# Optimization experiments

Measured on AMD Instinct MI355X. Metric: run time of the kernel, lower is better.

The kernel has to match this reference:

```python
import jax, jax.numpy as jnp
import numpy as np

EMBED_DIM = 1024
NUM_HEADS = 16
HEAD_DIM = EMBED_DIM // NUM_HEADS


def setup_inputs() -> dict:
    key = jax.random.key(0)
    ks = jax.random.split(key, 9)
    B, T, C = 4, 2048, EMBED_DIM
    s = 1.0 / np.sqrt(C)
    return {
        "x": jax.random.normal(ks[0], (B, T, C), jnp.float32),
        "Wq": jax.random.normal(ks[1], (C, C), jnp.float32) * s,
        "bq": jnp.zeros((C,), jnp.float32),
        "Wk": jax.random.normal(ks[2], (C, C), jnp.float32) * s,
        "bk": jnp.zeros((C,), jnp.float32),
        "Wv": jax.random.normal(ks[3], (C, C), jnp.float32) * s,
        "bv": jnp.zeros((C,), jnp.float32),
        "Wo": jax.random.normal(ks[4], (C, C), jnp.float32) * s,
        "bo": jnp.zeros((C,), jnp.float32),
    }


def reference(x, Wq, bq, Wk, bk, Wv, bv, Wo, bo):
    B, T, C = x.shape
    H, D = NUM_HEADS, HEAD_DIM
    # projections (torch Linear: y = x @ W.T + b; here weights stored as [in, out])
    q = (x @ Wq + bq).reshape(B, T, H, D).transpose(0, 2, 1, 3)  # [B,H,T,D]
    k = (x @ Wk + bk).reshape(B, T, H, D).transpose(0, 2, 1, 3)
    v = (x @ Wv + bv).reshape(B, T, H, D).transpose(0, 2, 1, 3)
    scores = jnp.einsum("bhqd,bhkd->bhqk", q, k) / jnp.sqrt(jnp.float32(D))
    causal = jnp.tril(jnp.ones((T, T), bool))
    scores = jnp.where(causal, scores, -jnp.inf)
    attn = jax.nn.softmax(scores, axis=-1)
    out = jnp.einsum("bhqk,bhkd->bhqd", attn, v)  # [B,H,T,D]
    out = out.transpose(0, 2, 1, 3).reshape(B, T, C)
    return out @ Wo + bo
```

## Files before the change

### kernel.cpp

```cpp
#include <hip/hip_runtime.h>
#include <hip/hip_bf16.h>
#include <math.h>

typedef __hip_bfloat16 bf16_t;
typedef __attribute__((ext_vector_type(8))) short short8;
typedef __attribute__((ext_vector_type(4))) float floatx4;

#define T_SEQ 2048
#define NB    4
#define NH    16
#define HD    64
#define C_DIM 1024
#define M_ROWS (NB * T_SEQ)

#define Q_SCALE 0.18033688011f

__device__ __forceinline__ void load_lds16(const bf16_t* g, bf16_t* l) {
    __builtin_amdgcn_global_load_lds(
        (const __attribute__((address_space(1))) void*)g,
        (__attribute__((address_space(3))) void*)l,
        16, 0, 0);
}

__device__ __forceinline__ floatx4 mfma16(short8 a, short8 b, floatx4 c) {
    return __builtin_amdgcn_mfma_f32_16x16x32_bf16(a, b, c, 0, 0, 0);
}

__global__ void convert_x_kernel(const float* __restrict__ x, bf16_t* __restrict__ xb) {
    int i = blockIdx.x * 256 + threadIdx.x;
    float4 v = reinterpret_cast<const float4*>(x)[i];
    union { bf16_t h[4]; short4 s4; } u;
    u.h[0] = __float2bfloat16(v.x);
    u.h[1] = __float2bfloat16(v.y);
    u.h[2] = __float2bfloat16(v.z);
    u.h[3] = __float2bfloat16(v.w);
    reinterpret_cast<short4*>(xb)[i] = u.s4;
}

__global__ void transpose_cvt_kernel(const float* __restrict__ W0, const float* __restrict__ W1,
                                     const float* __restrict__ W2, const float* __restrict__ W3,
                                     bf16_t* __restrict__ O0, bf16_t* __restrict__ O1,
                                     bf16_t* __restrict__ O2, bf16_t* __restrict__ O3) {
    const float* W = (blockIdx.z == 0) ? W0 : (blockIdx.z == 1) ? W1 : (blockIdx.z == 2) ? W2 : W3;
    bf16_t*      O = (blockIdx.z == 0) ? O0 : (blockIdx.z == 1) ? O1 : (blockIdx.z == 2) ? O2 : O3;
    __shared__ float tile[32][33];
    int bx = blockIdx.x * 32, by = blockIdx.y * 32;
    int tx = threadIdx.x, ty = threadIdx.y;
#pragma unroll
    for (int j = 0; j < 32; j += 8)
        tile[ty + j][tx] = W[(size_t)(by + ty + j) * C_DIM + bx + tx];
    __syncthreads();
#pragma unroll
    for (int j = 0; j < 32; j += 8)
        O[(size_t)(bx + ty + j) * C_DIM + by + tx] = __float2bfloat16(tile[tx][ty + j]);
}

__device__ __forceinline__ void gemm_mainloop(const bf16_t* __restrict__ Ablk,
                                              const bf16_t* __restrict__ Bblk,
                                              bf16_t* As, bf16_t* Bs,
                                              floatx4 acc[4][4], int wave, int lane) {
    int lr = lane & 15, lq = lane >> 4;
    int wr = (wave >> 1) * 64, wc = (wave & 1) * 64;
    for (int kt = 0; kt < C_DIM; kt += 64) {
#pragma unroll
        for (int j = 0; j < 4; ++j) {
            int chunk = j * 256 + wave * 64 + lane;
            int r = chunk >> 3, ps = chunk & 7;
            int c = ((ps ^ (r & 7)) * 8);
            load_lds16(Ablk + (size_t)r * C_DIM + kt + c, As + chunk * 8);
            load_lds16(Bblk + (size_t)r * C_DIM + kt + c, Bs + chunk * 8);
        }
        __syncthreads();
#pragma unroll
        for (int kk = 0; kk < 2; ++kk) {
            short8 af[4], bfr[4];
            int psw = ((kk * 4 + lq) ^ (lr & 7)) * 8;
#pragma unroll
            for (int m = 0; m < 4; ++m)
                af[m] = *reinterpret_cast<const short8*>(As + (wr + m * 16 + lr) * 64 + psw);
#pragma unroll
            for (int n = 0; n < 4; ++n)
                bfr[n] = *reinterpret_cast<const short8*>(Bs + (wc + n * 16 + lr) * 64 + psw);
#pragma unroll
            for (int m = 0; m < 4; ++m)
#pragma unroll
                for (int n = 0; n < 4; ++n)
                    acc[m][n] = mfma16(af[m], bfr[n], acc[m][n]);
        }
        __syncthreads();
    }
}

__global__ __launch_bounds__(256, 3) void gemm_qkv_kernel(
    const bf16_t* __restrict__ xb,
    const bf16_t* __restrict__ WqT, const bf16_t* __restrict__ WkT, const bf16_t* __restrict__ WvT,
    const float* __restrict__ bq, const float* __restrict__ bk, const float* __restrict__ bv,
    bf16_t* __restrict__ Q, bf16_t* __restrict__ K, bf16_t* __restrict__ Vt) {
    __shared__ bf16_t As[128 * 64];
    __shared__ bf16_t Bs[128 * 64];
    int tid = threadIdx.x, wave = tid >> 6, lane = tid & 63;

    int f    = (int)blockIdx.x + ((int)blockIdx.y << 3) + ((int)blockIdx.z << 9);
    int xcd  = f & 7;
    int s    = f >> 3;
    int rloc = s & 7;
    int t2   = s >> 3;
    int colp = t2 & 7;
    int wsel = t2 >> 3;
    int row0 = (xcd * 8 + rloc) * 128;
    int col0 = colp * 128;

    const bf16_t* Wt  = (wsel == 0) ? WqT : (wsel == 1) ? WkT : WvT;
    const float* bias = (wsel == 0) ? bq : (wsel == 1) ? bk : bv;

    floatx4 acc[4][4] = {};
    gemm_mainloop(xb + (size_t)row0 * C_DIM, Wt + (size_t)col0 * C_DIM, As, Bs, acc, wave, lane);

    int lr = lane & 15, lq = lane >> 4;
    int wr = (wave >> 1) * 64, wc = (wave & 1) * 64;

    if (wsel == 2) {
#pragma unroll
        for (int nt = 0; nt < 4; ++nt) {
            int col = col0 + wc + nt * 16 + lr;
            float bvv = bias[col];
            int h = col >> 6, d = col & 63;
#pragma unroll
            for (int m = 0; m < 4; ++m) {
                int rowg0 = row0 + wr + m * 16 + lq * 4;
                int b = rowg0 >> 11, t0 = rowg0 & (T_SEQ - 1);
                union { bf16_t h4[4]; short4 s4; } u;
#pragma unroll
                for (int r = 0; r < 4; ++r)
                    u.h4[r] = __float2bfloat16(acc[m][nt][r] + bvv);
                *reinterpret_cast<short4*>(
                    &Vt[((size_t)((b * NH + h) * HD + d)) * T_SEQ + t0]) = u.s4;
            }
        }
    } else {
        float scale = (wsel == 0) ? Q_SCALE : 1.0f;
        bf16_t* outp = (wsel == 0) ? Q : K;
#pragma unroll
        for (int nt = 0; nt < 4; ++nt) {
            int col = col0 + wc + nt * 16 + lr;
            float bvv = bias[col];
            int h = col >> 6, d = col & 63;
#pragma unroll
            for (int m = 0; m < 4; ++m) {
#pragma unroll
                for (int r = 0; r < 4; ++r) {
                    int rowg = row0 + wr + m * 16 + lq * 4 + r;
                    int b = rowg >> 11, t = rowg & (T_SEQ - 1);
                    float val = (acc[m][nt][r] + bvv) * scale;
                    outp[((size_t)((b * NH + h) * T_SEQ + t)) * HD + d] =
                        __float2bfloat16(val);
                }
            }
        }
    }
}

__global__ __launch_bounds__(256, 2) void attn_kernel(
    const bf16_t* __restrict__ Q, const bf16_t* __restrict__ K,
    const bf16_t* __restrict__ Vt, bf16_t* __restrict__ ctx) {
    __shared__ __align__(16) bf16_t Ks[2][64 * 64];
    __shared__ __align__(16) bf16_t Vs[2][64 * 64];
    __shared__ __align__(16) unsigned short Ps[128 * 64];
    int tid = threadIdx.x, w = tid >> 6, lane = tid & 63;
    int lr = lane & 15, lq = lane >> 4;
    int xcd = (int)blockIdx.x;
    int y   = (int)blockIdx.y;
    int bh  = xcd * 8 + (y & 7);
    int qp  = y >> 3;
    int b = bh >> 4, h = bh & 15;

    const bf16_t* Kbase = K  + (size_t)bh * T_SEQ * HD;
    const bf16_t* Vbase = Vt + (size_t)bh * HD * T_SEQ;

#pragma unroll 1
    for (int pass = 0; pass < 2; ++pass) {
        int qt = pass ? qp : (15 - qp);
        int q0 = qt * 128;
        int ktiles = 2 * qt + 2;
        const bf16_t* Qbase = Q + ((size_t)bh * T_SEQ + q0) * HD;

#pragma unroll
        for (int cc = 0; cc < 2; ++cc) {
            int ch = tid + cc * 256;
            int r = ch >> 3, ps = ch & 7;
            int c = ((ps ^ (r & 7)) * 8);
            load_lds16(Kbase + (size_t)r * HD + c, Ks[0] + ch * 8);
            load_lds16(Vbase + (size_t)r * T_SEQ + c, Vs[0] + ch * 8);
        }

        short8 qf[2][2];
#pragma unroll
        for (int g = 0; g < 2; ++g)
#pragma unroll
            for (int kk = 0; kk < 2; ++kk)
                qf[g][kk] = *reinterpret_cast<const short8*>(
                    Qbase + (size_t)(w * 32 + g * 16 + lr) * HD + kk * 32 + lq * 8);

        floatx4 o[2][4] = {};
        float lpart[2][4] = {};
        int buf = 0;

        for (int it = 0; it < ktiles; ++it) {
            int kt0 = it * 64;
            __syncthreads();

            if (it + 1 < ktiles) {
                int nk0 = kt0 + 64;
#pragma unroll
                for (int cc = 0; cc < 2; ++cc) {
                    int ch = tid + cc * 256;
                    int r = ch >> 3, ps = ch & 7;
                    int c = ((ps ^ (r & 7)) * 8);
                    load_lds16(Kbase + (size_t)(nk0 + r) * HD + c, Ks[buf ^ 1] + ch * 8);
                    load_lds16(Vbase + (size_t)r * T_SEQ + nk0 + c, Vs[buf ^ 1] + ch * 8);
                }
            }

            const bf16_t* Kc = Ks[buf];
            const bf16_t* Vc = Vs[buf];

            floatx4 s[2][4] = {};
            short8 kf[4][2];
#pragma unroll
            for (int kk = 0; kk < 2; ++kk) {
                int psw = ((kk * 4 + lq) ^ (lr & 7)) * 8;
#pragma unroll
                for (int n = 0; n < 4; ++n)
                    kf[n][kk] = *reinterpret_cast<const short8*>(Kc + (n * 16 + lr) * 64 + psw);
            }
#pragma unroll
            for (int g = 0; g < 2; ++g)
#pragma unroll
                for (int kk = 0; kk < 2; ++kk)
#pragma unroll
                    for (int n = 0; n < 4; ++n)
                        s[g][n] = mfma16(qf[g][kk], kf[n][kk], s[g][n]);

            if (it >= ktiles - 2) {
#pragma unroll
                for (int g = 0; g < 2; ++g)
#pragma unroll
                    for (int r = 0; r < 4; ++r) {
                        int rowg = q0 + w * 32 + g * 16 + lq * 4 + r;
#pragma unroll
                        for (int n = 0; n < 4; ++n) {
                            int colg = kt0 + n * 16 + lr;
                            if (colg > rowg) s[g][n][r] = -1e30f;
                        }
                    }
            }

#pragma unroll
            for (int g = 0; g < 2; ++g) {
#pragma unroll
                for (int n = 0; n < 4; ++n)
#pragma unroll
                    for (int r = 0; r < 4; ++r)
                        s[g][n][r] = __builtin_amdgcn_exp2f(s[g][n][r]);
#pragma unroll
                for (int r = 0; r < 4; ++r)
                    lpart[g][r] += (s[g][0][r] + s[g][1][r]) + (s[g][2][r] + s[g][3][r]);
            }

#pragma unroll
            for (int g = 0; g < 2; ++g)
#pragma unroll
                for (int n = 0; n < 4; ++n)
#pragma unroll
                    for (int r = 0; r < 4; ++r) {
                        int prow = w * 32 + g * 16 + lq * 4 + r;
                        int piece = n * 2 + (lr >> 3);
                        union { float f; unsigned u; } cv; cv.f = s[g][n][r];
                        Ps[prow * 64 + ((piece ^ (prow & 7)) * 8) + (lr & 7)] =
                            (unsigned short)(cv.u >> 16);
                    }

            short8 pf[2][2], vf[4][2];
#pragma unroll
            for (int g = 0; g < 2; ++g)
#pragma unroll
                for (int kk = 0; kk < 2; ++kk) {
                    int prow = w * 32 + g * 16 + lr;
                    pf[g][kk] = *reinterpret_cast<const short8*>(
                        Ps + prow * 64 + (((kk * 4 + lq) ^ (lr & 7)) * 8));
                }
#pragma unroll
            for (int kk = 0; kk < 2; ++kk) {
                int psw = ((kk * 4 + lq) ^ (lr & 7)) * 8;
#pragma unroll
                for (int dt = 0; dt < 4; ++dt)
                    vf[dt][kk] = *reinterpret_cast<const short8*>(Vc + (dt * 16 + lr) * 64 + psw);
            }
#pragma unroll
            for (int g = 0; g < 2; ++g)
#pragma unroll
                for (int kk = 0; kk < 2; ++kk)
#pragma unroll
                    for (int dt = 0; dt < 4; ++dt)
                        o[g][dt] = mfma16(pf[g][kk], vf[dt][kk], o[g][dt]);

            buf ^= 1;
        }

#pragma unroll
        for (int g = 0; g < 2; ++g)
#pragma unroll
            for (int r = 0; r < 4; ++r) {
                float l = lpart[g][r];
                l += __shfl_xor(l, 1);
                l += __shfl_xor(l, 2);
                l += __shfl_xor(l, 4);
                l += __shfl_xor(l, 8);
                float inv = 1.0f / l;
                int t = q0 + w * 32 + g * 16 + lq * 4 + r;
#pragma unroll
                for (int dt = 0; dt < 4; ++dt) {
                    int d = dt * 16 + lr;
                    ctx[((size_t)(b * T_SEQ + t)) * C_DIM + h * HD + d] =
                        __float2bfloat16(o[g][dt][r] * inv);
                }
            }
    }
}

__global__ __launch_bounds__(256, 3) void gemm_out_kernel(
    const bf16_t* __restrict__ Actx, const bf16_t* __restrict__ WoT,
    const float* __restrict__ bo, float* __restrict__ out) {
    __shared__ bf16_t As[128 * 64];
    __shared__ bf16_t Bs[128 * 64];
    int tid = threadIdx.x, wave = tid >> 6, lane = tid & 63;

    int f    = (int)blockIdx.x + ((int)blockIdx.y << 3);
    int xcd  = f & 7;
    int s    = f >> 3;
    int rloc = s & 7;
    int colp = s >> 3;
    int row0 = (xcd * 8 + rloc) * 128;
    int col0 = colp * 128;

    floatx4 acc[4][4] = {};
    gemm_mainloop(Actx + (size_t)row0 * C_DIM, WoT + (size_t)col0 * C_DIM, As, Bs, acc, wave, lane);
    int lr = lane & 15, lq = lane >> 4;
    int wr = (wave >> 1) * 64, wc = (wave & 1) * 64;
#pragma unroll
    for (int nt = 0; nt < 4; ++nt) {
        int col = col0 + wc + nt * 16 + lr;
        float bvv = bo[col];
#pragma unroll
        for (int m = 0; m < 4; ++m)
#pragma unroll
            for (int r = 0; r < 4; ++r) {
                int rowg = row0 + wr + m * 16 + lq * 4 + r;
                out[(size_t)rowg * C_DIM + col] = acc[m][nt][r] + bvv;
            }
    }
}

extern "C" void kernel_launch(void* const* d_in, const int* in_sizes, int n_in,
                              void* d_out, int out_size, void* d_ws, size_t ws_size,
                              hipStream_t stream) {
    const float* x  = (const float*)d_in[0];
    const float* Wq = (const float*)d_in[1];
    const float* bq = (const float*)d_in[2];
    const float* Wk = (const float*)d_in[3];
    const float* bk = (const float*)d_in[4];
    const float* Wv = (const float*)d_in[5];
    const float* bv = (const float*)d_in[6];
    const float* Wo = (const float*)d_in[7];
    const float* bo = (const float*)d_in[8];
    float* out = (float*)d_out;

    char* ws = (char*)d_ws;
    bf16_t* xb  = (bf16_t*)ws; ws += (size_t)M_ROWS * C_DIM * 2;
    bf16_t* WqT = (bf16_t*)ws; ws += (size_t)C_DIM * C_DIM * 2;
    bf16_t* WkT = (bf16_t*)ws; ws += (size_t)C_DIM * C_DIM * 2;
    bf16_t* WvT = (bf16_t*)ws; ws += (size_t)C_DIM * C_DIM * 2;
    bf16_t* WoT = (bf16_t*)ws; ws += (size_t)C_DIM * C_DIM * 2;
    bf16_t* Qb  = (bf16_t*)ws; ws += (size_t)M_ROWS * C_DIM * 2;
    bf16_t* Kb  = (bf16_t*)ws; ws += (size_t)M_ROWS * C_DIM * 2;
    bf16_t* Vtb = (bf16_t*)ws; ws += (size_t)M_ROWS * C_DIM * 2;
    bf16_t* ctx = (bf16_t*)ws; ws += (size_t)M_ROWS * C_DIM * 2;

    convert_x_kernel<<<(M_ROWS * C_DIM / 4) / 256, 256, 0, stream>>>(x, xb);
    transpose_cvt_kernel<<<dim3(32, 32, 4), dim3(32, 8), 0, stream>>>(
        Wq, Wk, Wv, Wo, WqT, WkT, WvT, WoT);
    gemm_qkv_kernel<<<dim3(8, 64, 3), 256, 0, stream>>>(
        xb, WqT, WkT, WvT, bq, bk, bv, Qb, Kb, Vtb);
    attn_kernel<<<dim3(8, 64), 256, 0, stream>>>(Qb, Kb, Vtb, ctx);
    gemm_out_kernel<<<dim3(8, 64), 256, 0, stream>>>(ctx, WoT, bo, out);
}
```

Baseline: 237.0 us.

## Compute S transposed and repack P in registers, widen KV tiles to 128

```diff
diff --git a/kernel.cpp b/kernel.cpp
--- a/kernel.cpp
+++ b/kernel.cpp
@@ -163,9 +163,8 @@
 __global__ __launch_bounds__(256, 2) void attn_kernel(
     const bf16_t* __restrict__ Q, const bf16_t* __restrict__ K,
     const bf16_t* __restrict__ Vt, bf16_t* __restrict__ ctx) {
-    __shared__ __align__(16) bf16_t Ks[2][64 * 64];
-    __shared__ __align__(16) bf16_t Vs[2][64 * 64];
-    __shared__ __align__(16) unsigned short Ps[128 * 64];
+    __shared__ __align__(16) bf16_t Ks[2][128 * 64];
+    __shared__ __align__(16) bf16_t Vs[2][64 * 128];
     int tid = threadIdx.x, w = tid >> 6, lane = tid & 63;
     int lr = lane & 15, lq = lane >> 4;
     int xcd = (int)blockIdx.x;
@@ -177,20 +176,26 @@
     const bf16_t* Kbase = K  + (size_t)bh * T_SEQ * HD;
     const bf16_t* Vbase = Vt + (size_t)bh * HD * T_SEQ;
 
+    int buf = 0;
 #pragma unroll 1
     for (int pass = 0; pass < 2; ++pass) {
         int qt = pass ? qp : (15 - qp);
         int q0 = qt * 128;
-        int ktiles = 2 * qt + 2;
+        int ktiles = qt + 1;
         const bf16_t* Qbase = Q + ((size_t)bh * T_SEQ + q0) * HD;
 
-#pragma unroll
-        for (int cc = 0; cc < 2; ++cc) {
-            int ch = tid + cc * 256;
-            int r = ch >> 3, ps = ch & 7;
-            int c = ((ps ^ (r & 7)) * 8);
-            load_lds16(Kbase + (size_t)r * HD + c, Ks[0] + ch * 8);
-            load_lds16(Vbase + (size_t)r * T_SEQ + c, Vs[0] + ch * 8);
+        {
+            int kt0s = 0;
+#pragma unroll
+            for (int cc = 0; cc < 4; ++cc) {
+                int ch = tid + cc * 256;
+                int r = ch >> 3, ps = ch & 7;
+                int c = (ps ^ (r & 7)) * 8;
+                load_lds16(Kbase + (size_t)(kt0s + r) * HD + c, Ks[buf] + ch * 8);
+                int rv = ch >> 4, pv = ch & 15;
+                int cv = (pv ^ (rv & 7)) * 8;
+                load_lds16(Vbase + (size_t)rv * T_SEQ + kt0s + cv, Vs[buf] + ch * 8);
+            }
         }
 
         short8 qf[2][2];
@@ -202,129 +207,142 @@
                     Qbase + (size_t)(w * 32 + g * 16 + lr) * HD + kk * 32 + lq * 8);
 
         floatx4 o[2][4] = {};
-        float lpart[2][4] = {};
-        int buf = 0;
+        float lpart[2] = {0.f, 0.f};
 
         for (int it = 0; it < ktiles; ++it) {
-            int kt0 = it * 64;
             __syncthreads();
 
             if (it + 1 < ktiles) {
-                int nk0 = kt0 + 64;
-#pragma unroll
-                for (int cc = 0; cc < 2; ++cc) {
+                int nk0 = (it + 1) * 128;
+#pragma unroll
+                for (int cc = 0; cc < 4; ++cc) {
                     int ch = tid + cc * 256;
                     int r = ch >> 3, ps = ch & 7;
-                    int c = ((ps ^ (r & 7)) * 8);
+                    int c = (ps ^ (r & 7)) * 8;
                     load_lds16(Kbase + (size_t)(nk0 + r) * HD + c, Ks[buf ^ 1] + ch * 8);
-                    load_lds16(Vbase + (size_t)r * T_SEQ + nk0 + c, Vs[buf ^ 1] + ch * 8);
+                    int rv = ch >> 4, pv = ch & 15;
+                    int cv = (pv ^ (rv & 7)) * 8;
+                    load_lds16(Vbase + (size_t)rv * T_SEQ + nk0 + cv, Vs[buf ^ 1] + ch * 8);
                 }
             }
 
             const bf16_t* Kc = Ks[buf];
             const bf16_t* Vc = Vs[buf];
-
-            floatx4 s[2][4] = {};
-            short8 kf[4][2];
-#pragma unroll
-            for (int kk = 0; kk < 2; ++kk) {
-                int psw = ((kk * 4 + lq) ^ (lr & 7)) * 8;
-#pragma unroll
-                for (int n = 0; n < 4; ++n)
-                    kf[n][kk] = *reinterpret_cast<const short8*>(Kc + (n * 16 + lr) * 64 + psw);
-            }
-#pragma unroll
-            for (int g = 0; g < 2; ++g)
-#pragma unroll
-                for (int kk = 0; kk < 2; ++kk)
+            bool last = (it == ktiles - 1);
+
+#pragma unroll
+            for (int sub = 0; sub < 2; ++sub) {
+                int ktb = it * 128 + sub * 64;
+
+                floatx4 s[2][4] = {};
+                {
+                    short8 kf[4][2];
+#pragma unroll
+                    for (int kk = 0; kk < 2; ++kk) {
+                        int psw = ((kk * 4 + lq) ^ (lr & 7)) * 8;
+#pragma unroll
+                        for (int n = 0; n < 4; ++n)
+                            kf[n][kk] = *reinterpret_cast<const short8*>(
+                                Kc + (sub * 64 + n * 16 + lr) * 64 + psw);
+                    }
+#pragma unroll
+                    for (int g = 0; g < 2; ++g)
+#pragma unroll
+                        for (int kk = 0; kk < 2; ++kk)
+#pragma unroll
+                            for (int n = 0; n < 4; ++n)
+                                s[g][n] = mfma16(kf[n][kk], qf[g][kk], s[g][n]);
+                }
+
+                if (last) {
+#pragma unroll
+                    for (int g = 0; g < 2; ++g) {
+                        int rowg = q0 + w * 32 + g * 16 + lr;
+#pragma unroll
+                        for (int n = 0; n < 4; ++n)
+#pragma unroll
+                            for (int r = 0; r < 4; ++r) {
+                                int colg = ktb + n * 16 + lq * 4 + r;
+                                if (colg > rowg) s[g][n][r] = -1e30f;
+                            }
+                    }
+                }
+
+                short8 pf[2][2];
+#pragma unroll
+                for (int g = 0; g < 2; ++g) {
 #pragma unroll
                     for (int n = 0; n < 4; ++n)
-                        s[g][n] = mfma16(qf[g][kk], kf[n][kk], s[g][n]);
-
-            if (it >= ktiles - 2) {
+#pragma unroll
+                        for (int r = 0; r < 4; ++r)
+                            s[g][n][r] = __builtin_amdgcn_exp2f(s[g][n][r]);
+                    float p0 = (s[g][0][0] + s[g][0][1]) + (s[g][0][2] + s[g][0][3]);
+                    float p1 = (s[g][1][0] + s[g][1][1]) + (s[g][1][2] + s[g][1][3]);
+                    float p2 = (s[g][2][0] + s[g][2][1]) + (s[g][2][2] + s[g][2][3]);
+                    float p3 = (s[g][3][0] + s[g][3][1]) + (s[g][3][2] + s[g][3][3]);
+                    lpart[g] += (p0 + p1) + (p2 + p3);
+
+                    unsigned upk[4][2];
+#pragma unroll
+                    for (int n = 0; n < 4; ++n) {
+                        asm("v_cvt_pk_bf16_f32 %0, %1, %2"
+                            : "=v"(upk[n][0]) : "v"(s[g][n][0]), "v"(s[g][n][1]));
+                        asm("v_cvt_pk_bf16_f32 %0, %1, %2"
+                            : "=v"(upk[n][1]) : "v"(s[g][n][2]), "v"(s[g][n][3]));
+                    }
+#pragma unroll
+                    for (int kk = 0; kk < 2; ++kk) {
+                        unsigned x0 = upk[2 * kk][0], y0 = upk[2 * kk + 1][0];
+                        unsigned x1 = upk[2 * kk][1], y1 = upk[2 * kk + 1][1];
+                        asm("v_permlane32_swap_b32 %0, %1" : "+v"(x0), "+v"(y0));
+                        asm("v_permlane32_swap_b32 %0, %1" : "+v"(x1), "+v"(y1));
+                        asm("v_permlane16_swap_b32 %0, %1" : "+v"(x0), "+v"(y0));
+                        asm("v_permlane16_swap_b32 %0, %1" : "+v"(x1), "+v"(y1));
+                        union { unsigned u4[4]; short8 s8; } pk;
+                        pk.u4[0] = x0; pk.u4[1] = x1; pk.u4[2] = y0; pk.u4[3] = y1;
+                        pf[g][kk] = pk.s8;
+                    }
+                }
+
+                short8 vf[4][2];
+#pragma unroll
+                for (int kk = 0; kk < 2; ++kk) {
+                    int psw = ((sub * 8 + kk * 4 + lq) ^ (lr & 7)) * 8;
+#pragma unroll
+                    for (int dt = 0; dt < 4; ++dt)
+                        vf[dt][kk] = *reinterpret_cast<const short8*>(
+                            Vc + (dt * 16 + lr) * 128 + psw);
+                }
 #pragma unroll
                 for (int g = 0; g < 2; ++g)
 #pragma unroll
-                    for (int r = 0; r < 4; ++r) {
-                        int rowg = q0 + w * 32 + g * 16 + lq * 4 + r;
-#pragma unroll
-                        for (int n = 0; n < 4; ++n) {
-                            int colg = kt0 + n * 16 + lr;
-                            if (colg > rowg) s[g][n][r] = -1e30f;
-                        }
-                    }
-            }
-
-#pragma unroll
-            for (int g = 0; g < 2; ++g) {
-#pragma unroll
-                for (int n = 0; n < 4; ++n)
-#pragma unroll
-                    for (int r = 0; r < 4; ++r)
-                        s[g][n][r] = __builtin_amdgcn_exp2f(s[g][n][r]);
-#pragma unroll
-                for (int r = 0; r < 4; ++r)
-                    lpart[g][r] += (s[g][0][r] + s[g][1][r]) + (s[g][2][r] + s[g][3][r]);
-            }
-
-#pragma unroll
-            for (int g = 0; g < 2; ++g)
-#pragma unroll
-                for (int n = 0; n < 4; ++n)
-#pragma unroll
-                    for (int r = 0; r < 4; ++r) {
-                        int prow = w * 32 + g * 16 + lq * 4 + r;
-                        int piece = n * 2 + (lr >> 3);
-                        union { float f; unsigned u; } cv; cv.f = s[g][n][r];
-                        Ps[prow * 64 + ((piece ^ (prow & 7)) * 8) + (lr & 7)] =
-                            (unsigned short)(cv.u >> 16);
-                    }
-
-            short8 pf[2][2], vf[4][2];
-#pragma unroll
-            for (int g = 0; g < 2; ++g)
-#pragma unroll
-                for (int kk = 0; kk < 2; ++kk) {
-                    int prow = w * 32 + g * 16 + lr;
-                    pf[g][kk] = *reinterpret_cast<const short8*>(
-                        Ps + prow * 64 + (((kk * 4 + lq) ^ (lr & 7)) * 8));
-                }
-#pragma unroll
-            for (int kk = 0; kk < 2; ++kk) {
-                int psw = ((kk * 4 + lq) ^ (lr & 7)) * 8;
-#pragma unroll
-                for (int dt = 0; dt < 4; ++dt)
-                    vf[dt][kk] = *reinterpret_cast<const short8*>(Vc + (dt * 16 + lr) * 64 + psw);
-            }
-#pragma unroll
-            for (int g = 0; g < 2; ++g)
-#pragma unroll
-                for (int kk = 0; kk < 2; ++kk)
-#pragma unroll
-                    for (int dt = 0; dt < 4; ++dt)
-                        o[g][dt] = mfma16(pf[g][kk], vf[dt][kk], o[g][dt]);
+                    for (int kk = 0; kk < 2; ++kk)
+#pragma unroll
+                        for (int dt = 0; dt < 4; ++dt)
+                            o[g][dt] = mfma16(pf[g][kk], vf[dt][kk], o[g][dt]);
+            }
 
             buf ^= 1;
         }
 
 #pragma unroll
-        for (int g = 0; g < 2; ++g)
+        for (int g = 0; g < 2; ++g) {
+            float l = lpart[g];
+            l += __shfl_xor(l, 16);
+            l += __shfl_xor(l, 32);
+            float inv = 1.0f / l;
 #pragma unroll
             for (int r = 0; r < 4; ++r) {
-                float l = lpart[g][r];
-                l += __shfl_xor(l, 1);
-                l += __shfl_xor(l, 2);
-                l += __shfl_xor(l, 4);
-                l += __shfl_xor(l, 8);
-                float inv = 1.0f / l;
+                float invr = __shfl(inv, (lane & 48) | (lq * 4 + r));
                 int t = q0 + w * 32 + g * 16 + lq * 4 + r;
 #pragma unroll
                 for (int dt = 0; dt < 4; ++dt) {
                     int d = dt * 16 + lr;
                     ctx[((size_t)(b * T_SEQ + t)) * C_DIM + h * HD + d] =
-                        __float2bfloat16(o[g][dt][r] * inv);
-                }
-            }
+                        __float2bfloat16(o[g][dt][r] * invr);
+                }
+            }
+        }
     }
 }
 
```

Result: faster. 230.9 us (-2.6%).
